# Optimization experiments

Hardware: AMD Instinct MI355X
Metric: run time of the kernel (lower is better)

## Reference

```python
import jax, jax.numpy as jnp
import numpy as np

FP4_MAX = 6.0  # largest E2M1 magnitude


def _round_fp4(y):
    # Round to nearest value on the FP4 E2M1 grid {0, +-0.5, 1, 1.5, 2, 3, 4, 6}.
    a = jnp.abs(y)
    e = jnp.floor(jnp.log2(jnp.maximum(a, 1.0)))  # 0 for a<2, 1 for [2,4), 2 for >=4
    step = jnp.exp2(e - 1.0)                      # grid spacing: 0.5, 1, 2
    q = jnp.clip(jnp.round(a / step) * step, 0.0, FP4_MAX)
    return jnp.sign(y) * q


def _ste_round_fp4(y):
    # straight-through estimator: identity gradient through the rounding
    return y + jax.lax.stop_gradient(_round_fp4(y) - y)


def _mxfp4_quant(x, group_size, eps=None):
    # Groupwise MXFP4 quant-dequant along the last axis.
    lead, d = x.shape[:-1], x.shape[-1]
    g = d // group_size
    xg = x.reshape(lead + (g, group_size))
    amax = jnp.max(jnp.abs(xg), axis=-1, keepdims=True)
    # shared exponent per MX spec: floor(log2(amax)) - emax_elem (emax_elem = 2 for FP4)
    exps = jnp.where(amax > 0.0,
                     jnp.floor(jnp.log2(jnp.maximum(amax, 1e-30))) - 2.0,
                     0.0)
    scale = jnp.exp2(exps)
    if eps is not None:
        # learnable (adversarially perturbed) per-group scale epsilon
        scale = scale * (1.0 + eps[..., None])
    y = xg / scale
    xq = _ste_round_fp4(y) * scale
    return xq.reshape(x.shape), jnp.squeeze(exps, -1)


def setup_inputs() -> dict:
    key = jax.random.key(0)
    ks = jax.random.split(key, 4)
    B, S, DIN, DOUT, GS = 4, 2048, 4096, 4096, 32
    x = jax.random.normal(ks[0], (B, S, DIN), jnp.float32)
    weight_fp = jax.random.normal(ks[1], (DOUT, DIN), jnp.float32) * 0.02  # frozen FP weight
    bias = jax.random.normal(ks[2], (DOUT,), jnp.float32) * 0.01
    eps = jnp.zeros((DOUT, DIN // GS), jnp.float32)  # learnable weight-quant epsilon
    adversarial_delta = jax.random.normal(ks[3], (DOUT, DIN // GS), jnp.float32) * 0.01
    return {"x": x, "adversarial_delta": adversarial_delta,
            "weight_fp": weight_fp, "bias": bias, "eps": eps}


def reference(x, adversarial_delta, weight_fp, bias, eps):
    GS = 32
    # dynamic activation MXFP4 quantization
    x_q, act_exps = _mxfp4_quant(x, GS)
    # weight MXFP4 quantization with learnable + adversarial epsilon
    eps_eff = eps + adversarial_delta
    w_q, w_exps = _mxfp4_quant(weight_fp, GS, eps_eff)
    # F.linear(x_q, w_q, bias)
    out = jnp.einsum('bsi,oi->bso', x_q, w_q) + bias
    return (out, eps_eff, w_exps, act_exps)
```

## Files before the change

kernel.cpp:

```cpp
#include <hip/hip_runtime.h>
#include <hip/hip_bf16.h>

#define DIN   4096
#define DOUT  4096
#define MROWS 8192
#define GSIZE 32
#define NGPR  (DIN / GSIZE)
#define NG_ACT (MROWS * NGPR)
#define NG_W   (DOUT * NGPR)

typedef __bf16 bf16_t;
typedef __attribute__((ext_vector_type(8))) __bf16 bf16x8;
typedef __attribute__((ext_vector_type(4))) float f32x4;

typedef const __attribute__((address_space(1))) void* gptr_t;
typedef __attribute__((address_space(3))) void* lptr_t;

__device__ __forceinline__ float fp4_round(float y) {
  float a  = __builtin_fabsf(y);
  float am = fmaxf(a, 1.0f);
  int   e  = (int)((__float_as_uint(am) >> 23) & 255u) - 127;
  float step = __uint_as_float((unsigned)(e - 1 + 127) << 23);
  float q = rintf(a / step) * step;
  q = fminf(q, 6.0f);
  return copysignf(q, y);
}

__global__ __launch_bounds__(256) void act_quant(const float* __restrict__ x,
                                                 bf16_t* __restrict__ xq,
                                                 float* __restrict__ exps_out) {
  int g = blockIdx.x * 256 + threadIdx.x;
  const float4* xp = reinterpret_cast<const float4*>(x) + (size_t)g * 8;
  float v[32];
  float amax = 0.f;
#pragma unroll
  for (int i = 0; i < 8; ++i) {
    float4 t = xp[i];
    v[4*i+0] = t.x; v[4*i+1] = t.y; v[4*i+2] = t.z; v[4*i+3] = t.w;
    amax = fmaxf(amax, fmaxf(fmaxf(__builtin_fabsf(t.x), __builtin_fabsf(t.y)),
                             fmaxf(__builtin_fabsf(t.z), __builtin_fabsf(t.w))));
  }
  float exps = 0.f;
  if (amax > 0.f) {
    float am = fmaxf(amax, 1e-30f);
    exps = (float)((int)((__float_as_uint(am) >> 23) & 255u) - 129);
  }
  float scale = __uint_as_float((unsigned)((int)exps + 127) << 23);
  float inv   = __uint_as_float((unsigned)(127 - (int)exps) << 23);
  bf16x8 hv[4];
#pragma unroll
  for (int i = 0; i < 32; ++i) {
    float q = fp4_round(v[i] * inv) * scale;
    hv[i >> 3][i & 7] = (bf16_t)q;
  }
  bf16x8* dst = reinterpret_cast<bf16x8*>(xq + (size_t)g * 32);
#pragma unroll
  for (int i = 0; i < 4; ++i) dst[i] = hv[i];
  exps_out[g] = exps;
}

__global__ __launch_bounds__(256) void w_quant(const float* __restrict__ w,
                                               const float* __restrict__ eps,
                                               const float* __restrict__ adv,
                                               bf16_t* __restrict__ wq,
                                               float* __restrict__ eps_eff_out,
                                               float* __restrict__ w_exps_out) {
  int g = blockIdx.x * 256 + threadIdx.x;
  float ee = eps[g] + adv[g];
  eps_eff_out[g] = ee;
  const float4* wp = reinterpret_cast<const float4*>(w) + (size_t)g * 8;
  float v[32];
  float amax = 0.f;
#pragma unroll
  for (int i = 0; i < 8; ++i) {
    float4 t = wp[i];
    v[4*i+0] = t.x; v[4*i+1] = t.y; v[4*i+2] = t.z; v[4*i+3] = t.w;
    amax = fmaxf(amax, fmaxf(fmaxf(__builtin_fabsf(t.x), __builtin_fabsf(t.y)),
                             fmaxf(__builtin_fabsf(t.z), __builtin_fabsf(t.w))));
  }
  float exps = 0.f;
  if (amax > 0.f) {
    float am = fmaxf(amax, 1e-30f);
    exps = (float)((int)((__float_as_uint(am) >> 23) & 255u) - 129);
  }
  w_exps_out[g] = exps;
  float p2   = __uint_as_float((unsigned)((int)exps + 127) << 23);
  float scale = p2 * (1.0f + ee);
  bf16x8 hv[4];
#pragma unroll
  for (int i = 0; i < 32; ++i) {
    float q = fp4_round(v[i] / scale) * scale;
    hv[i >> 3][i & 7] = (bf16_t)q;
  }
  bf16x8* dst = reinterpret_cast<bf16x8*>(wq + (size_t)g * 32);
#pragma unroll
  for (int i = 0; i < 4; ++i) dst[i] = hv[i];
}

#define NT 64

__global__ __launch_bounds__(512, 2) void gemm_bt(const bf16_t* __restrict__ A,
                                                  const bf16_t* __restrict__ B,
                                                  const float* __restrict__ bias,
                                                  float* __restrict__ C) {
  __shared__ bf16_t sA[2 * 16384];
  __shared__ bf16_t sB[2 * 16384];
  const int tid  = threadIdx.x;
  const int wave = tid >> 6;
  const int lane = tid & 63;

  const int swz = (blockIdx.x & 7) * 64 + (blockIdx.x >> 3);
  const int tm0 = (swz >> 4) * 256;
  const int tn0 = (swz & 15) * 256;

  const int wr = wave >> 2;
  const int wc = wave & 3;

  const int lrow8 = lane >> 3;
  const int csw   = ((lane & 7) ^ lrow8) * 8;
  const bf16_t* gA = A + (size_t)(tm0 + wave * 16 + lrow8) * DIN + csw;
  const bf16_t* gB = B + (size_t)(tn0 + wave * 16 + lrow8) * DIN + csw;
  const int stg0 = wave * 1024;

#define STGH(sM, gM, d, h, kt) do {                                          \
    const bf16_t* g_ = (gM) + (size_t)(h) * 128 * DIN + (size_t)(kt) * 64;   \
    __builtin_amdgcn_global_load_lds((gptr_t)g_,                             \
        (lptr_t)((sM) + (d) * 16384 + (h) * 8192 + stg0), 16, 0, 0);         \
    __builtin_amdgcn_global_load_lds((gptr_t)(g_ + 8 * DIN),                 \
        (lptr_t)((sM) + (d) * 16384 + (h) * 8192 + stg0 + 512), 16, 0, 0);   \
  } while (0)

  const int arow_b = (wr * 128 + (lane & 15)) * 128;
  const int brow_b = (wc * 64 + (lane & 15)) * 128;
  const int slot0  = (((lane >> 4) ^ (lane & 7)) << 4);

  f32x4 acc[8][4] = {};

  STGH(sA, gA, 0, 0, 0); STGH(sA, gA, 0, 1, 0);
  STGH(sB, gB, 0, 0, 0); STGH(sB, gB, 0, 1, 0);
  STGH(sB, gB, 1, 0, 1); STGH(sB, gB, 1, 1, 1);
  STGH(sA, gA, 1, 0, 1); STGH(sA, gA, 1, 1, 1);
  asm volatile("s_waitcnt vmcnt(8)" ::: "memory");
  asm volatile("s_barrier" ::: "memory");

  for (int j = 0; j < NT; ++j) {
    const int p = j & 1;
    const char* bufA = (const char*)sA + p * 32768;
    const char* bufB = (const char*)sB + p * 32768;
    bf16x8 a0[4][2], a1[4][2], bn[4][2];

#pragma unroll
    for (int m = 0; m < 4; ++m)
#pragma unroll
      for (int kk = 0; kk < 2; ++kk)
        a0[m][kk] = *reinterpret_cast<const bf16x8*>(bufA + arow_b + m * 2048 + (slot0 ^ (kk << 6)));
#pragma unroll
    for (int t = 0; t < 2; ++t)
#pragma unroll
      for (int kk = 0; kk < 2; ++kk)
        bn[t][kk] = *reinterpret_cast<const bf16x8*>(bufB + brow_b + t * 2048 + (slot0 ^ (kk << 6)));
    asm volatile("s_barrier" ::: "memory");
    asm volatile("s_waitcnt lgkmcnt(0)" ::: "memory");
    __builtin_amdgcn_s_setprio(1);
#pragma unroll
    for (int kk = 0; kk < 2; ++kk)
#pragma unroll
      for (int t = 0; t < 2; ++t)
#pragma unroll
        for (int m = 0; m < 4; ++m)
          acc[m][t] = __builtin_amdgcn_mfma_f32_16x16x32_bf16(a0[m][kk], bn[t][kk], acc[m][t], 0, 0, 0);
    __builtin_amdgcn_s_setprio(0);
    asm volatile("s_barrier" ::: "memory");

#pragma unroll
    for (int t = 2; t < 4; ++t)
#pragma unroll
      for (int kk = 0; kk < 2; ++kk)
        bn[t][kk] = *reinterpret_cast<const bf16x8*>(bufB + brow_b + t * 2048 + (slot0 ^ (kk << 6)));
    asm volatile("s_barrier" ::: "memory");
    asm volatile("s_waitcnt lgkmcnt(0)" ::: "memory");
    __builtin_amdgcn_s_setprio(1);
#pragma unroll
    for (int kk = 0; kk < 2; ++kk)
#pragma unroll
      for (int t = 0; t < 2; ++t)
#pragma unroll
        for (int m = 0; m < 4; ++m)
          acc[m][2 + t] = __builtin_amdgcn_mfma_f32_16x16x32_bf16(a0[m][kk], bn[2 + t][kk], acc[m][2 + t], 0, 0, 0);
    __builtin_amdgcn_s_setprio(0);
    asm volatile("s_barrier" ::: "memory");

#pragma unroll
    for (int m = 0; m < 4; ++m)
#pragma unroll
      for (int kk = 0; kk < 2; ++kk)
        a1[m][kk] = *reinterpret_cast<const bf16x8*>(bufA + arow_b + (4 + m) * 2048 + (slot0 ^ (kk << 6)));
    if (j + 2 < NT) {
      STGH(sB, gB, p, 0, j + 2);
      STGH(sB, gB, p, 1, j + 2);
    }
    asm volatile("s_barrier" ::: "memory");
    asm volatile("s_waitcnt lgkmcnt(0)" ::: "memory");
    __builtin_amdgcn_s_setprio(1);
#pragma unroll
    for (int kk = 0; kk < 2; ++kk)
#pragma unroll
      for (int t = 0; t < 2; ++t)
#pragma unroll
        for (int m = 0; m < 4; ++m)
          acc[4 + m][t] = __builtin_amdgcn_mfma_f32_16x16x32_bf16(a1[m][kk], bn[t][kk], acc[4 + m][t], 0, 0, 0);
    __builtin_amdgcn_s_setprio(0);
    asm volatile("s_barrier" ::: "memory");

    if (j + 2 < NT) {
      STGH(sA, gA, p, 0, j + 2);
      STGH(sA, gA, p, 1, j + 2);
    }
    asm volatile("s_barrier" ::: "memory");
    __builtin_amdgcn_s_setprio(1);
#pragma unroll
    for (int kk = 0; kk < 2; ++kk)
#pragma unroll
      for (int t = 0; t < 2; ++t)
#pragma unroll
        for (int m = 0; m < 4; ++m)
          acc[4 + m][2 + t] = __builtin_amdgcn_mfma_f32_16x16x32_bf16(a1[m][kk], bn[2 + t][kk], acc[4 + m][2 + t], 0, 0, 0);
    __builtin_amdgcn_s_setprio(0);
    if (j < NT - 2) {
      asm volatile("s_waitcnt vmcnt(8)" ::: "memory");
    } else {
      asm volatile("s_waitcnt vmcnt(0)" ::: "memory");
    }
    asm volatile("s_barrier" ::: "memory");
  }

  const int r0 = tm0 + wr * 128 + ((lane >> 4) << 2);
  const int c0 = tn0 + wc * 64 + (lane & 15);
#pragma unroll
  for (int n = 0; n < 4; ++n) {
    float bv = bias[c0 + n * 16];
#pragma unroll
    for (int m = 0; m < 8; ++m) {
#pragma unroll
      for (int jj = 0; jj < 4; ++jj) {
        C[(size_t)(r0 + m * 16 + jj) * DOUT + c0 + n * 16] = acc[m][n][jj] + bv;
      }
    }
  }
#undef STGH
}

extern "C" void kernel_launch(void* const* d_in, const int* in_sizes, int n_in,
                              void* d_out, int out_size, void* d_ws, size_t ws_size,
                              hipStream_t stream) {
  const float* x    = (const float*)d_in[0];
  const float* adv  = (const float*)d_in[1];
  const float* wfp  = (const float*)d_in[2];
  const float* bias = (const float*)d_in[3];
  const float* eps  = (const float*)d_in[4];

  float* out      = (float*)d_out;
  float* eps_eff  = out + (size_t)MROWS * DOUT;
  float* w_exps   = eps_eff + NG_W;
  float* act_exps = w_exps + NG_W;

  bf16_t* xq = (bf16_t*)d_ws;
  bf16_t* wq = (bf16_t*)d_ws + (size_t)MROWS * DIN;

  act_quant<<<NG_ACT / 256, 256, 0, stream>>>(x, xq, act_exps);
  w_quant<<<NG_W / 256, 256, 0, stream>>>(wfp, eps, adv, wq, eps_eff, w_exps);
  gemm_bt<<<dim3((MROWS / 256) * (DOUT / 256)), 512, 0, stream>>>(xq, wq, bias, out);
}
```

Before: 352.1 us.

## Reorder GEMM main loop phases and interleave B prefetch one tile ahead

Restructures the bf16 MFMA main loop so the B tile for the next iteration is prefetched one step ahead, split across the first two phases, while the A tile stays two steps ahead. The four MFMA phases are reordered (a0·b01, a1·b01, a0·b23, a1·b23) so each phase issues one half-tile of global-to-LDS loads, and the vmcnt waits are relaxed. Memory clobbers are dropped from the waitcnt and barrier asm. The aim is to spread global loads more evenly across the loop and overlap them with compute. The tighter B lookahead and the dropped clobbers risk exposing more load latency or allowing compiler reordering across the waits.

```diff
diff --git a/kernel.cpp b/kernel.cpp
--- a/kernel.cpp
+++ b/kernel.cpp
@@ -138,10 +138,9 @@
 
   STGH(sA, gA, 0, 0, 0); STGH(sA, gA, 0, 1, 0);
   STGH(sB, gB, 0, 0, 0); STGH(sB, gB, 0, 1, 0);
-  STGH(sB, gB, 1, 0, 1); STGH(sB, gB, 1, 1, 1);
   STGH(sA, gA, 1, 0, 1); STGH(sA, gA, 1, 1, 1);
-  asm volatile("s_waitcnt vmcnt(8)" ::: "memory");
-  asm volatile("s_barrier" ::: "memory");
+  asm volatile("s_waitcnt vmcnt(4)");
+  __builtin_amdgcn_s_barrier();
 
   for (int j = 0; j < NT; ++j) {
     const int p = j & 1;
@@ -159,8 +158,10 @@
 #pragma unroll
       for (int kk = 0; kk < 2; ++kk)
         bn[t][kk] = *reinterpret_cast<const bf16x8*>(bufB + brow_b + t * 2048 + (slot0 ^ (kk << 6)));
-    asm volatile("s_barrier" ::: "memory");
-    asm volatile("s_waitcnt lgkmcnt(0)" ::: "memory");
+    if (j + 1 < NT) STGH(sB, gB, p ^ 1, 0, j + 1);
+    asm volatile("s_waitcnt lgkmcnt(8)");
+    __builtin_amdgcn_s_barrier();
+    asm volatile("s_waitcnt lgkmcnt(0)");
     __builtin_amdgcn_s_setprio(1);
 #pragma unroll
     for (int kk = 0; kk < 2; ++kk)
@@ -170,15 +171,35 @@
         for (int m = 0; m < 4; ++m)
           acc[m][t] = __builtin_amdgcn_mfma_f32_16x16x32_bf16(a0[m][kk], bn[t][kk], acc[m][t], 0, 0, 0);
     __builtin_amdgcn_s_setprio(0);
-    asm volatile("s_barrier" ::: "memory");
+    __builtin_amdgcn_s_barrier();
+
+#pragma unroll
+    for (int m = 0; m < 4; ++m)
+#pragma unroll
+      for (int kk = 0; kk < 2; ++kk)
+        a1[m][kk] = *reinterpret_cast<const bf16x8*>(bufA + arow_b + (4 + m) * 2048 + (slot0 ^ (kk << 6)));
+    if (j + 1 < NT) STGH(sB, gB, p ^ 1, 1, j + 1);
+    __builtin_amdgcn_s_barrier();
+    asm volatile("s_waitcnt lgkmcnt(0)");
+    __builtin_amdgcn_s_setprio(1);
+#pragma unroll
+    for (int kk = 0; kk < 2; ++kk)
+#pragma unroll
+      for (int t = 0; t < 2; ++t)
+#pragma unroll
+        for (int m = 0; m < 4; ++m)
+          acc[4 + m][t] = __builtin_amdgcn_mfma_f32_16x16x32_bf16(a1[m][kk], bn[t][kk], acc[4 + m][t], 0, 0, 0);
+    __builtin_amdgcn_s_setprio(0);
+    __builtin_amdgcn_s_barrier();
 
 #pragma unroll
     for (int t = 2; t < 4; ++t)
 #pragma unroll
       for (int kk = 0; kk < 2; ++kk)
         bn[t][kk] = *reinterpret_cast<const bf16x8*>(bufB + brow_b + t * 2048 + (slot0 ^ (kk << 6)));
-    asm volatile("s_barrier" ::: "memory");
-    asm volatile("s_waitcnt lgkmcnt(0)" ::: "memory");
+    if (j + 2 < NT) STGH(sA, gA, p, 0, j + 2);
+    __builtin_amdgcn_s_barrier();
+    asm volatile("s_waitcnt lgkmcnt(0)");
     __builtin_amdgcn_s_setprio(1);
 #pragma unroll
     for (int kk = 0; kk < 2; ++kk)
@@ -188,50 +209,26 @@
         for (int m = 0; m < 4; ++m)
           acc[m][2 + t] = __builtin_amdgcn_mfma_f32_16x16x32_bf16(a0[m][kk], bn[2 + t][kk], acc[m][2 + t], 0, 0, 0);
     __builtin_amdgcn_s_setprio(0);
-    asm volatile("s_barrier" ::: "memory");
-
-#pragma unroll
-    for (int m = 0; m < 4; ++m)
-#pragma unroll
-      for (int kk = 0; kk < 2; ++kk)
-        a1[m][kk] = *reinterpret_cast<const bf16x8*>(bufA + arow_b + (4 + m) * 2048 + (slot0 ^ (kk << 6)));
-    if (j + 2 < NT) {
-      STGH(sB, gB, p, 0, j + 2);
-      STGH(sB, gB, p, 1, j + 2);
+    __builtin_amdgcn_s_barrier();
+
+    if (j + 2 < NT) STGH(sA, gA, p, 1, j + 2);
+    __builtin_amdgcn_s_barrier();
+    asm volatile("s_waitcnt lgkmcnt(0)");
+    __builtin_amdgcn_s_setprio(1);
+#pragma unroll
+    for (int kk = 0; kk < 2; ++kk)
+#pragma unroll
+      for (int t = 0; t < 2; ++t)
+#pragma unroll
+        for (int m = 0; m < 4; ++m)
+          acc[4 + m][2 + t] = __builtin_amdgcn_mfma_f32_16x16x32_bf16(a1[m][kk], bn[2 + t][kk], acc[4 + m][2 + t], 0, 0, 0);
+    __builtin_amdgcn_s_setprio(0);
+    if (j < NT - 2) {
+      asm volatile("s_waitcnt vmcnt(4)");
+    } else {
+      asm volatile("s_waitcnt vmcnt(0)");
     }
-    asm volatile("s_barrier" ::: "memory");
-    asm volatile("s_waitcnt lgkmcnt(0)" ::: "memory");
-    __builtin_amdgcn_s_setprio(1);
-#pragma unroll
-    for (int kk = 0; kk < 2; ++kk)
-#pragma unroll
-      for (int t = 0; t < 2; ++t)
-#pragma unroll
-        for (int m = 0; m < 4; ++m)
-          acc[4 + m][t] = __builtin_amdgcn_mfma_f32_16x16x32_bf16(a1[m][kk], bn[t][kk], acc[4 + m][t], 0, 0, 0);
-    __builtin_amdgcn_s_setprio(0);
-    asm volatile("s_barrier" ::: "memory");
-
-    if (j + 2 < NT) {
-      STGH(sA, gA, p, 0, j + 2);
-      STGH(sA, gA, p, 1, j + 2);
-    }
-    asm volatile("s_barrier" ::: "memory");
-    __builtin_amdgcn_s_setprio(1);
-#pragma unroll
-    for (int kk = 0; kk < 2; ++kk)
-#pragma unroll
-      for (int t = 0; t < 2; ++t)
-#pragma unroll
-        for (int m = 0; m < 4; ++m)
-          acc[4 + m][2 + t] = __builtin_amdgcn_mfma_f32_16x16x32_bf16(a1[m][kk], bn[2 + t][kk], acc[4 + m][2 + t], 0, 0, 0);
-    __builtin_amdgcn_s_setprio(0);
-    if (j < NT - 2) {
-      asm volatile("s_waitcnt vmcnt(8)" ::: "memory");
-    } else {
-      asm volatile("s_waitcnt vmcnt(0)" ::: "memory");
-    }
-    asm volatile("s_barrier" ::: "memory");
+    __builtin_amdgcn_s_barrier();
   }
 
   const int r0 = tm0 + wr * 128 + ((lane >> 4) << 2);
```

New measurement: 373.7 us. 1.06x slower.
